# Performance work log

Measured on AMD Instinct MI355X. Metric: run time of the kernel, lower is better.

## Reference

```python
import jax, jax.numpy as jnp
import numpy as np

NEG_SLOPE = 0.2

def gat_layer(x, W, al, ar, src, dst, n_dst):
    # x: [Ns, Fin]; W: [Fin, H*D]; al/ar: [H, D]; src/dst: [E]
    H, D = al.shape
    h = (x @ W).reshape(-1, H, D)          # [Ns, H, D]
    h_dst = h[:n_dst]                       # dst nodes are prefix of src nodes (DGL block)
    el = (h * al).sum(-1)                   # [Ns, H]
    er = (h_dst * ar).sum(-1)               # [Nd, H]
    e = jax.nn.leaky_relu(el[src] + er[dst], NEG_SLOPE)  # [E, H]
    m = jax.ops.segment_max(e, dst, num_segments=n_dst)  # stable edge-softmax
    a = jnp.exp(e - m[dst])
    s = jax.ops.segment_sum(a, dst, num_segments=n_dst)
    alpha = a / s[dst]                      # [E, H]
    msg = h[src] * alpha[:, :, None]        # [E, H, D]
    out = jax.ops.segment_sum(msg, dst, num_segments=n_dst)  # [Nd, H, D]
    return out.reshape(n_dst, H * D)


def setup_inputs() -> dict:
    key = jax.random.key(0)
    ks = jax.random.split(key, 16)
    N0, N1, N2, N3 = 200000, 100000, 50000, 25000
    E0, E1, E2 = 1000000, 500000, 250000
    Fin, Dh, H, C = 256, 64, 3, 40
    inp = {}
    inp['x'] = jax.random.normal(ks[0], (N0, Fin), jnp.float32)
    inp['src0'] = jax.random.randint(ks[1], (E0,), 0, N0, jnp.int32)
    inp['dst0'] = jnp.sort(jax.random.randint(ks[2], (E0,), 0, N1, jnp.int32))
    inp['src1'] = jax.random.randint(ks[3], (E1,), 0, N1, jnp.int32)
    inp['dst1'] = jnp.sort(jax.random.randint(ks[4], (E1,), 0, N2, jnp.int32))
    inp['src2'] = jax.random.randint(ks[5], (E2,), 0, N2, jnp.int32)
    inp['dst2'] = jnp.sort(jax.random.randint(ks[6], (E2,), 0, N3, jnp.int32))
    sc = lambda f: np.float32(1.0 / np.sqrt(f))
    inp['W0'] = jax.random.normal(ks[7], (Fin, H * Dh), jnp.float32) * sc(Fin)
    inp['al0'] = jax.random.normal(ks[8], (H, Dh), jnp.float32) * sc(Dh)
    inp['ar0'] = jax.random.normal(ks[9], (H, Dh), jnp.float32) * sc(Dh)
    inp['W1'] = jax.random.normal(ks[10], (H * Dh, H * Dh), jnp.float32) * sc(H * Dh)
    inp['al1'] = jax.random.normal(ks[11], (H, Dh), jnp.float32) * sc(Dh)
    inp['ar1'] = jax.random.normal(ks[12], (H, Dh), jnp.float32) * sc(Dh)
    inp['W2'] = jax.random.normal(ks[13], (H * Dh, C), jnp.float32) * sc(H * Dh)
    inp['al2'] = jax.random.normal(ks[14], (1, C), jnp.float32) * sc(C)
    inp['ar2'] = jax.random.normal(ks[15], (1, C), jnp.float32) * sc(C)
    return inp


def reference(x, src0, dst0, src1, dst1, src2, dst2,
              W0, al0, ar0, W1, al1, ar1, W2, al2, ar2):
    N1, N2, N3 = 100000, 50000, 25000
    h = gat_layer(x, W0, al0, ar0, src0, dst0, N1)
    h = jax.nn.relu(h)  # dropout is identity in eval/deterministic mode
    h = gat_layer(h, W1, al1, ar1, src1, dst1, N2)
    h = jax.nn.relu(h)
    out = gat_layer(h, W2, al2, ar2, src2, dst2, N3)  # [N3, n_classes]
    return out
```

## Files before the change

kernel.cpp:

```cpp
#include <hip/hip_runtime.h>
#include <math.h>

#define DEV_INLINE __device__ __forceinline__

typedef __attribute__((ext_vector_type(8))) short short8v;
typedef __attribute__((ext_vector_type(4))) float float4v;

DEV_INLINE unsigned short f2bf_rtn(float f) {
  unsigned u = __float_as_uint(f);
  u += 0x7FFFu + ((u >> 16) & 1u);
  return (unsigned short)(u >> 16);
}
DEV_INLINE float bf2f(unsigned short s) { return __uint_as_float(((unsigned)s) << 16); }

DEV_INLINE int soff(int row, int oct) { return row * 32 + ((oct ^ (row & 3)) << 3); }

__global__ void conv_w_all(const float* __restrict__ W0, const float* __restrict__ W1,
                           const float* __restrict__ W2, short* __restrict__ w0h,
                           short* __restrict__ w0l, short* __restrict__ w1h,
                           short* __restrict__ w1l, short* __restrict__ w2h,
                           short* __restrict__ w2l) {
  const int S0 = 256 * 192, S1 = 192 * 192, S2 = 192 * 40;
  int idx = blockIdx.x * 256 + threadIdx.x;
  const float* W; short *Wh, *Wl; int K;
  if (idx < S0) { W = W0; Wh = w0h; Wl = w0l; K = 256; }
  else if (idx < S0 + S1) { idx -= S0; W = W1; Wh = w1h; Wl = w1l; K = 192; }
  else if (idx < S0 + S1 + S2) { idx -= S0 + S1; W = W2; Wh = w2h; Wl = w2l; K = 192; }
  else return;
  int n = idx / K, k = idx - n * K;
  int N = (W == W0 || W == W1) ? 192 : 40;
  float w = W[(size_t)k * N + n];
  unsigned short h = f2bf_rtn(w);
  Wh[idx] = (short)h;
  Wl[idx] = (short)f2bf_rtn(w - bf2f(h));
}

__global__ void csr_all(const int* __restrict__ d0, const int* __restrict__ d1,
                        const int* __restrict__ d2, int* __restrict__ o0,
                        int* __restrict__ o1, int* __restrict__ o2,
                        int E0, int E1, int E2, int n1, int n2, int n3) {
  int i = blockIdx.x * 256 + threadIdx.x;
  const int* dst; int* off; int E, nd;
  if (i < E0) { dst = d0; off = o0; E = E0; nd = n1; }
  else if (i < E0 + E1) { i -= E0; dst = d1; off = o1; E = E1; nd = n2; }
  else if (i < E0 + E1 + E2) { i -= E0 + E1; dst = d2; off = o2; E = E2; nd = n3; }
  else return;
  int d = dst[i];
  int p = (i == 0) ? -1 : dst[i - 1];
  for (int q = p + 1; q <= d; ++q) off[q] = i;
  if (i == E - 1)
    for (int q = d + 1; q <= nd; ++q) off[q] = E;
}

template <int NT, int H>
__global__ __launch_bounds__(256) void gemm_fused(
    const float* __restrict__ A, const short* __restrict__ Bth,
    const short* __restrict__ Btl, const float* __restrict__ al,
    const float* __restrict__ ar, float* __restrict__ C,
    float* __restrict__ el, float* __restrict__ er,
    int M, int N, int K, int n_dst) {
  constexpr int BN = NT * 16;
  constexpr int BREP = (BN + 63) / 64;
  constexpr int TPH = NT / H;
  __shared__ short As_h[128 * 32], As_l[128 * 32];
  __shared__ short Bs_h[BN * 32], Bs_l[BN * 32];
  const int tid = threadIdx.x;
  const int w = tid >> 6, lane = tid & 63;
  const int quad = lane >> 4, l16 = lane & 15;
  const int m0 = blockIdx.x * 128;

  float4v acc[2][NT];
#pragma unroll
  for (int mt = 0; mt < 2; ++mt)
#pragma unroll
    for (int nt = 0; nt < NT; ++nt)
#pragma unroll
      for (int r = 0; r < 4; ++r) acc[mt][nt][r] = 0.f;

  const int sr = tid >> 2;
  const int oct = tid & 3;

  for (int k0 = 0; k0 < K; k0 += 32) {
    float4 a0[2], a1[2];
#pragma unroll
    for (int p = 0; p < 2; ++p) {
      int gr = m0 + sr + p * 64;
      if (gr < M) {
        const float* ap = A + (size_t)gr * K + k0 + oct * 8;
        a0[p] = *(const float4*)ap;
        a1[p] = *(const float4*)(ap + 4);
      } else {
        a0[p] = make_float4(0.f, 0.f, 0.f, 0.f);
        a1[p] = a0[p];
      }
    }
    short8v bh[BREP], bl[BREP];
#pragma unroll
    for (int q = 0; q < BREP; ++q) {
      int n = sr + q * 64;
      if (n < BN) {
        if (n < N) {
          bh[q] = *(const short8v*)(Bth + (size_t)n * K + k0 + oct * 8);
          bl[q] = *(const short8v*)(Btl + (size_t)n * K + k0 + oct * 8);
        } else {
#pragma unroll
          for (int j = 0; j < 8; ++j) { bh[q][j] = 0; bl[q][j] = 0; }
        }
      }
    }
    __syncthreads();
#pragma unroll
    for (int p = 0; p < 2; ++p) {
      int r = sr + p * 64;
      float vs[8] = {a0[p].x, a0[p].y, a0[p].z, a0[p].w,
                     a1[p].x, a1[p].y, a1[p].z, a1[p].w};
      short8v hv, lv;
#pragma unroll
      for (int j = 0; j < 8; ++j) {
        unsigned short h = f2bf_rtn(vs[j]);
        hv[j] = (short)h;
        lv[j] = (short)f2bf_rtn(vs[j] - bf2f(h));
      }
      *(short8v*)(As_h + soff(r, oct)) = hv;
      *(short8v*)(As_l + soff(r, oct)) = lv;
    }
#pragma unroll
    for (int q = 0; q < BREP; ++q) {
      int n = sr + q * 64;
      if (n < BN) {
        *(short8v*)(Bs_h + soff(n, oct)) = bh[q];
        *(short8v*)(Bs_l + soff(n, oct)) = bl[q];
      }
    }
    __syncthreads();
    short8v afh[2], afl[2];
#pragma unroll
    for (int mt = 0; mt < 2; ++mt) {
      int row = w * 32 + mt * 16 + l16;
      afh[mt] = *(const short8v*)(As_h + soff(row, quad));
      afl[mt] = *(const short8v*)(As_l + soff(row, quad));
    }
#pragma unroll
    for (int nt = 0; nt < NT; ++nt) {
      int col = nt * 16 + l16;
      short8v bfh = *(const short8v*)(Bs_h + soff(col, quad));
      short8v bfl = *(const short8v*)(Bs_l + soff(col, quad));
#pragma unroll
      for (int mt = 0; mt < 2; ++mt) {
        acc[mt][nt] = __builtin_amdgcn_mfma_f32_16x16x32_bf16(afh[mt], bfh, acc[mt][nt], 0, 0, 0);
        acc[mt][nt] = __builtin_amdgcn_mfma_f32_16x16x32_bf16(afh[mt], bfl, acc[mt][nt], 0, 0, 0);
        acc[mt][nt] = __builtin_amdgcn_mfma_f32_16x16x32_bf16(afl[mt], bfh, acc[mt][nt], 0, 0, 0);
      }
    }
  }

  float av[NT], rv[NT];
#pragma unroll
  for (int nt = 0; nt < NT; ++nt) {
    int col = nt * 16 + l16;
    av[nt] = (col < N) ? al[col] : 0.f;
    rv[nt] = (col < N) ? ar[col] : 0.f;
  }
#pragma unroll
  for (int mt = 0; mt < 2; ++mt)
#pragma unroll
    for (int r = 0; r < 4; ++r) {
      int gm = m0 + w * 32 + mt * 16 + quad * 4 + r;
      if (gm >= M) continue;
      float pl[H], pr[H];
#pragma unroll
      for (int h = 0; h < H; ++h) { pl[h] = 0.f; pr[h] = 0.f; }
#pragma unroll
      for (int nt = 0; nt < NT; ++nt) {
        int h = nt / TPH;
        pl[h] = fmaf(acc[mt][nt][r], av[nt], pl[h]);
        pr[h] = fmaf(acc[mt][nt][r], rv[nt], pr[h]);
      }
#pragma unroll
      for (int h = 0; h < H; ++h) {
#pragma unroll
        for (int o = 8; o >= 1; o >>= 1) {
          pl[h] += __shfl_xor(pl[h], o, 16);
          pr[h] += __shfl_xor(pr[h], o, 16);
        }
      }
      if (l16 == 0) {
#pragma unroll
        for (int h = 0; h < H; ++h) {
          el[gm * H + h] = pl[h];
          if (gm < n_dst) er[gm * H + h] = pr[h];
        }
      }
#pragma unroll
      for (int nt = 0; nt < NT; ++nt) {
        int col = nt * 16 + l16;
        if (col < N) C[(size_t)gm * N + col] = acc[mt][nt][r];
      }
    }
}

template <int H, int D, bool RELU>
__global__ __launch_bounds__(256) void agg2_kernel(
    const float* __restrict__ hsrc, const float* __restrict__ el,
    const float* __restrict__ er, const int* __restrict__ src,
    const int* __restrict__ off, float* __restrict__ out, int n_dst) {
  constexpr int F = H * D;
  constexpr int NP = (F + 63) / 64;
  __shared__ float wbuf[16][16][H];
  __shared__ int sbuf[16][16];
  const int g = threadIdx.x >> 4, l = threadIdx.x & 15;
  const int d = blockIdx.x * 16 + g;
  if (d >= n_dst) return;
  const int lo = off[d], hi = off[d + 1];

  if (hi <= lo) {
#pragma unroll
    for (int p = 0; p < NP; ++p) {
      int c4 = (p * 16 + l) * 4;
      if (c4 < F) *(float4*)(out + (size_t)d * F + c4) = make_float4(0.f, 0.f, 0.f, 0.f);
    }
    return;
  }

  float erv[H], s_part[H];
#pragma unroll
  for (int h = 0; h < H; ++h) {
    erv[h] = er[d * H + h];
    s_part[h] = 0.f;
  }
  float4 acc[NP];
#pragma unroll
  for (int p = 0; p < NP; ++p) acc[p] = make_float4(0.f, 0.f, 0.f, 0.f);

  for (int base = lo; base < hi; base += 16) {
    const int i = base + l;
    const bool valid = i < hi;
    const int sid = valid ? src[i] : 0;
#pragma unroll
    for (int h = 0; h < H; ++h) {
      float e = 0.f;
      if (valid) {
        e = el[sid * H + h] + erv[h];
        e = e > 0.f ? e : 0.2f * e;
        e = __expf(e);
      }
      s_part[h] += e;
      wbuf[g][l][h] = e;
    }
    sbuf[g][l] = sid;

    const int cnt = min(16, hi - base);
    int sj = sbuf[g][0];
    float4 hv[NP], hn[NP];
#pragma unroll
    for (int p = 0; p < NP; ++p) {
      int c4 = (p * 16 + l) * 4;
      hv[p] = (c4 < F) ? *(const float4*)(hsrc + (size_t)sj * F + c4)
                       : make_float4(0.f, 0.f, 0.f, 0.f);
    }
    for (int ei = 0; ei < cnt; ++ei) {
      if (ei + 1 < cnt) {
        int sj2 = sbuf[g][ei + 1];
#pragma unroll
        for (int p = 0; p < NP; ++p) {
          int c4 = (p * 16 + l) * 4;
          hn[p] = (c4 < F) ? *(const float4*)(hsrc + (size_t)sj2 * F + c4)
                           : make_float4(0.f, 0.f, 0.f, 0.f);
        }
      }
#pragma unroll
      for (int p = 0; p < NP; ++p) {
        int c4 = (p * 16 + l) * 4;
        float wc = wbuf[g][ei][c4 / D];
        acc[p].x = fmaf(wc, hv[p].x, acc[p].x);
        acc[p].y = fmaf(wc, hv[p].y, acc[p].y);
        acc[p].z = fmaf(wc, hv[p].z, acc[p].z);
        acc[p].w = fmaf(wc, hv[p].w, acc[p].w);
      }
#pragma unroll
      for (int p = 0; p < NP; ++p) hv[p] = hn[p];
    }
  }

#pragma unroll
  for (int h = 0; h < H; ++h)
#pragma unroll
    for (int o = 8; o >= 1; o >>= 1) s_part[h] += __shfl_xor(s_part[h], o, 16);

#pragma unroll
  for (int p = 0; p < NP; ++p) {
    int c4 = (p * 16 + l) * 4;
    if (c4 < F) {
      float inv = 1.f / s_part[c4 / D];
      float4 o;
      o.x = acc[p].x * inv; o.y = acc[p].y * inv;
      o.z = acc[p].z * inv; o.w = acc[p].w * inv;
      if (RELU) {
        o.x = fmaxf(o.x, 0.f); o.y = fmaxf(o.y, 0.f);
        o.z = fmaxf(o.z, 0.f); o.w = fmaxf(o.w, 0.f);
      }
      *(float4*)(out + (size_t)d * F + c4) = o;
    }
  }
}

extern "C" void kernel_launch(void* const* d_in, const int* in_sizes, int n_in,
                              void* d_out, int out_size, void* d_ws, size_t ws_size,
                              hipStream_t stream) {
  const float* x   = (const float*)d_in[0];
  const int* src0  = (const int*)d_in[1];
  const int* dst0  = (const int*)d_in[2];
  const int* src1  = (const int*)d_in[3];
  const int* dst1  = (const int*)d_in[4];
  const int* src2  = (const int*)d_in[5];
  const int* dst2  = (const int*)d_in[6];
  const float* W0  = (const float*)d_in[7];
  const float* al0 = (const float*)d_in[8];
  const float* ar0 = (const float*)d_in[9];
  const float* W1  = (const float*)d_in[10];
  const float* al1 = (const float*)d_in[11];
  const float* ar1 = (const float*)d_in[12];
  const float* W2  = (const float*)d_in[13];
  const float* al2 = (const float*)d_in[14];
  const float* ar2 = (const float*)d_in[15];

  const int N0 = 200000, N1 = 100000, N2 = 50000, N3 = 25000;
  const int E0 = in_sizes[1], E1 = in_sizes[3], E2 = in_sizes[5];
  const int Fin = 256, F = 192, C = 40;

  float* ws     = (float*)d_ws;
  float* h_buf  = ws;
  float* o_buf  = h_buf + (size_t)N0 * F;
  float* el_buf = o_buf + (size_t)N1 * F;
  float* er_buf = el_buf + (size_t)N0 * 3;
  short* w0h    = (short*)(er_buf + (size_t)N1 * 3);
  short* w0l    = w0h + 192 * 256;
  short* w1h    = w0l + 192 * 256;
  short* w1l    = w1h + 192 * 192;
  short* w2h    = w1l + 192 * 192;
  short* w2l    = w2h + 40 * 192;
  int*   off0   = (int*)(w2l + 40 * 192);
  int*   off1   = off0 + (N1 + 1);
  int*   off2   = off1 + (N2 + 1);

  dim3 blk(256);

  const int WTOT = 256 * 192 + 192 * 192 + 192 * 40;
  conv_w_all<<<dim3((WTOT + 255) / 256), blk, 0, stream>>>(W0, W1, W2, w0h, w0l, w1h, w1l, w2h, w2l);
  const int ETOT = E0 + E1 + E2;
  csr_all<<<dim3((ETOT + 255) / 256), blk, 0, stream>>>(dst0, dst1, dst2, off0, off1, off2,
                                                        E0, E1, E2, N1, N2, N3);

  gemm_fused<12, 3><<<dim3((N0 + 127) / 128), blk, 0, stream>>>(
      x, w0h, w0l, al0, ar0, h_buf, el_buf, er_buf, N0, F, Fin, N1);
  agg2_kernel<3, 64, true><<<dim3((N1 + 15) / 16), blk, 0, stream>>>(
      h_buf, el_buf, er_buf, src0, off0, o_buf, N1);

  gemm_fused<12, 3><<<dim3((N1 + 127) / 128), blk, 0, stream>>>(
      o_buf, w1h, w1l, al1, ar1, h_buf, el_buf, er_buf, N1, F, F, N2);
  agg2_kernel<3, 64, true><<<dim3((N2 + 15) / 16), blk, 0, stream>>>(
      h_buf, el_buf, er_buf, src1, off1, o_buf, N2);

  gemm_fused<3, 1><<<dim3((N2 + 127) / 128), blk, 0, stream>>>(
      o_buf, w2h, w2l, al2, ar2, h_buf, el_buf, er_buf, N2, C, F, N3);
  agg2_kernel<1, 40, false><<<dim3((N3 + 15) / 16), blk, 0, stream>>>(
      h_buf, el_buf, er_buf, src2, off2, (float*)d_out, N3);
}
```

Measured before the change: 644.0 us.

## Prefetch next K-tile into registers, retune LDS swizzle and occupancy hint

The fused GEMM now issues global loads for the next K-slice right after the shared-memory stores, so the loads overlap the current slice's MFMA work instead of being serialized before it. The LDS swizzle XOR now uses (row>>1)&3 rather than row&3, aiming to reduce bank conflicts on the 16-byte fragment reads. The launch bounds add a minimum of 3 blocks per SM, which may cap registers and cause spills given the extra prefetch registers.

```diff
diff --git a/kernel.cpp b/kernel.cpp
--- a/kernel.cpp
+++ b/kernel.cpp
@@ -13,7 +13,7 @@
 }
 DEV_INLINE float bf2f(unsigned short s) { return __uint_as_float(((unsigned)s) << 16); }
 
-DEV_INLINE int soff(int row, int oct) { return row * 32 + ((oct ^ (row & 3)) << 3); }
+DEV_INLINE int soff(int row, int oct) { return row * 32 + ((oct ^ ((row >> 1) & 3)) << 3); }
 
 __global__ void conv_w_all(const float* __restrict__ W0, const float* __restrict__ W1,
                            const float* __restrict__ W2, short* __restrict__ w0h,
@@ -53,7 +53,7 @@
 }
 
 template <int NT, int H>
-__global__ __launch_bounds__(256) void gemm_fused(
+__global__ __launch_bounds__(256, 3) void gemm_fused(
     const float* __restrict__ A, const short* __restrict__ Bth,
     const short* __restrict__ Btl, const float* __restrict__ al,
     const float* __restrict__ ar, float* __restrict__ C,
@@ -80,40 +80,47 @@
   const int sr = tid >> 2;
   const int oct = tid & 3;
 
-  for (int k0 = 0; k0 < K; k0 += 32) {
-    float4 a0[2], a1[2];
+  float4 pa0[2], pa1[2];
+  short8v pbh[BREP], pbl[BREP];
+
+  auto issue = [&](int k0) {
 #pragma unroll
     for (int p = 0; p < 2; ++p) {
       int gr = m0 + sr + p * 64;
       if (gr < M) {
         const float* ap = A + (size_t)gr * K + k0 + oct * 8;
-        a0[p] = *(const float4*)ap;
-        a1[p] = *(const float4*)(ap + 4);
+        pa0[p] = *(const float4*)ap;
+        pa1[p] = *(const float4*)(ap + 4);
       } else {
-        a0[p] = make_float4(0.f, 0.f, 0.f, 0.f);
-        a1[p] = a0[p];
-      }
-    }
-    short8v bh[BREP], bl[BREP];
+        pa0[p] = make_float4(0.f, 0.f, 0.f, 0.f);
+        pa1[p] = pa0[p];
+      }
+    }
 #pragma unroll
     for (int q = 0; q < BREP; ++q) {
       int n = sr + q * 64;
       if (n < BN) {
         if (n < N) {
-          bh[q] = *(const short8v*)(Bth + (size_t)n * K + k0 + oct * 8);
-          bl[q] = *(const short8v*)(Btl + (size_t)n * K + k0 + oct * 8);
+          pbh[q] = *(const short8v*)(Bth + (size_t)n * K + k0 + oct * 8);
+          pbl[q] = *(const short8v*)(Btl + (size_t)n * K + k0 + oct * 8);
         } else {
 #pragma unroll
-          for (int j = 0; j < 8; ++j) { bh[q][j] = 0; bl[q][j] = 0; }
+          for (int j = 0; j < 8; ++j) { pbh[q][j] = 0; pbl[q][j] = 0; }
         }
       }
     }
+  };
+
+  issue(0);
+
+  const int nk = K >> 5;
+  for (int kt = 0; kt < nk; ++kt) {
     __syncthreads();
 #pragma unroll
     for (int p = 0; p < 2; ++p) {
       int r = sr + p * 64;
-      float vs[8] = {a0[p].x, a0[p].y, a0[p].z, a0[p].w,
-                     a1[p].x, a1[p].y, a1[p].z, a1[p].w};
+      float vs[8] = {pa0[p].x, pa0[p].y, pa0[p].z, pa0[p].w,
+                     pa1[p].x, pa1[p].y, pa1[p].z, pa1[p].w};
       short8v hv, lv;
 #pragma unroll
       for (int j = 0; j < 8; ++j) {
@@ -128,11 +135,12 @@
     for (int q = 0; q < BREP; ++q) {
       int n = sr + q * 64;
       if (n < BN) {
-        *(short8v*)(Bs_h + soff(n, oct)) = bh[q];
-        *(short8v*)(Bs_l + soff(n, oct)) = bl[q];
+        *(short8v*)(Bs_h + soff(n, oct)) = pbh[q];
+        *(short8v*)(Bs_l + soff(n, oct)) = pbl[q];
       }
     }
     __syncthreads();
+    if (kt + 1 < nk) issue((kt + 1) << 5);
     short8v afh[2], afl[2];
 #pragma unroll
     for (int mt = 0; mt < 2; ++mt) {
```

Result: slower. 840.1 us (+30.5%).
